# Kernel optimization log

Hardware: AMD Instinct MI355X
Metric: run time of the kernel (lower is better)

Reference implementation:

```python
import jax, jax.numpy as jnp
import numpy as np

N_ETYPES = 6
N_STEPS = 5
N_ITERS = 6
N_LSTM_LAYERS = 3
NODES_PER_GRAPH = 200


def _uinit(key, shape, fan_in):
    s = 1.0 / np.sqrt(fan_in)
    return jax.random.uniform(key, shape, jnp.float32, -s, s)


def setup_inputs() -> dict:
    key = jax.random.key(0)
    ks = jax.random.split(key, 24)
    N, D = 64000, 64
    G = N // NODES_PER_GRAPH  # 320 graphs
    E = N * 16  # 1,024,000 edges
    feats = jax.random.normal(ks[0], (N, D), jnp.float32)
    # within-graph edges: local endpoint + graph offset
    graph_of_edge = jnp.repeat(jnp.arange(G, dtype=jnp.int32), E // G)
    src = jax.random.randint(ks[1], (E,), 0, NODES_PER_GRAPH, jnp.int32) + graph_of_edge * NODES_PER_GRAPH
    dst = jax.random.randint(ks[2], (E,), 0, NODES_PER_GRAPH, jnp.int32) + graph_of_edge * NODES_PER_GRAPH
    etypes = jax.random.randint(ks[3], (E,), 0, N_ETYPES, jnp.int32)
    node_graph = jnp.repeat(jnp.arange(G, dtype=jnp.int32), NODES_PER_GRAPH)
    # GatedGraphConv params: per-etype Linear(D,D) + GRUCell(D,D) (torch gate order r,z,n)
    W_edge = _uinit(ks[4], (N_ETYPES, D, D), D)
    b_edge = _uinit(ks[5], (N_ETYPES, D), D)
    gru_W_ih = _uinit(ks[6], (3 * D, D), D)
    gru_W_hh = _uinit(ks[7], (3 * D, D), D)
    gru_b_ih = _uinit(ks[8], (3 * D,), D)
    gru_b_hh = _uinit(ks[9], (3 * D,), D)
    # Set2Set LSTM: 3 layers, input 2D (layer0) / D (layers 1,2), hidden D; torch gate order i,f,g,o
    lstm_W_ih0 = _uinit(ks[10], (4 * D, 2 * D), D)
    lstm_W_hh0 = _uinit(ks[11], (4 * D, D), D)
    lstm_b_ih0 = _uinit(ks[12], (4 * D,), D)
    lstm_b_hh0 = _uinit(ks[13], (4 * D,), D)
    lstm_W_ih1 = _uinit(ks[14], (4 * D, D), D)
    lstm_W_hh1 = _uinit(ks[15], (4 * D, D), D)
    lstm_b_ih1 = _uinit(ks[16], (4 * D,), D)
    lstm_b_hh1 = _uinit(ks[17], (4 * D,), D)
    lstm_W_ih2 = _uinit(ks[18], (4 * D, D), D)
    lstm_W_hh2 = _uinit(ks[19], (4 * D, D), D)
    lstm_b_ih2 = _uinit(ks[20], (4 * D,), D)
    lstm_b_hh2 = _uinit(ks[21], (4 * D,), D)
    Wp = _uinit(ks[22], (3, 2 * D), 2 * D)
    bp = _uinit(ks[23], (3,), 2 * D)
    return dict(feats=feats, W_edge=W_edge, b_edge=b_edge,
                gru_W_ih=gru_W_ih, gru_W_hh=gru_W_hh, gru_b_ih=gru_b_ih, gru_b_hh=gru_b_hh,
                lstm_W_ih0=lstm_W_ih0, lstm_W_hh0=lstm_W_hh0, lstm_b_ih0=lstm_b_ih0, lstm_b_hh0=lstm_b_hh0,
                lstm_W_ih1=lstm_W_ih1, lstm_W_hh1=lstm_W_hh1, lstm_b_ih1=lstm_b_ih1, lstm_b_hh1=lstm_b_hh1,
                lstm_W_ih2=lstm_W_ih2, lstm_W_hh2=lstm_W_hh2, lstm_b_ih2=lstm_b_ih2, lstm_b_hh2=lstm_b_hh2,
                Wp=Wp, bp=bp, src=src, dst=dst, etypes=etypes, node_graph=node_graph)


def _ggnn_forward(feats, W_edge, b_edge, gru_W_ih, gru_W_hh, gru_b_ih, gru_b_hh,
                  lstm_params, Wp, bp, src, dst, etypes, node_graph):
    N, D = feats.shape
    G = N // NODES_PER_GRAPH
    h = feats
    # --- GatedGraphConv: 5 steps of etype-typed transform + scatter-sum + GRU ---
    for _ in range(N_STEPS):
        # transform every node by every etype weight (cheap: N << E), then gather per edge
        Wh = jnp.einsum('nd,tdo->tno', h, W_edge) + b_edge[:, None, :]  # [T,N,D]
        msg = Wh[etypes, src]                                           # [E,D] gather
        a = jax.ops.segment_sum(msg, dst, num_segments=N)               # [N,D] scatter-add
        gi = a @ gru_W_ih.T + gru_b_ih
        gh = h @ gru_W_hh.T + gru_b_hh
        i_r, i_z, i_n = jnp.split(gi, 3, -1)
        h_r, h_z, h_n = jnp.split(gh, 3, -1)
        r = jax.nn.sigmoid(i_r + h_r)
        z = jax.nn.sigmoid(i_z + h_z)
        n = jnp.tanh(i_n + r * h_n)
        h = (1.0 - z) * n + z * h
    feat = h
    # --- Set2Set readout ---
    q_star = jnp.zeros((G, 2 * D), feat.dtype)
    hs = jnp.zeros((N_LSTM_LAYERS, G, D), feat.dtype)
    cs = jnp.zeros((N_LSTM_LAYERS, G, D), feat.dtype)
    for _ in range(N_ITERS):
        x = q_star
        new_h, new_c = [], []
        for l, (Wi, Whh, bi, bh) in enumerate(lstm_params):
            gates = x @ Wi.T + bi + hs[l] @ Whh.T + bh
            ii, ff, gg, oo = jnp.split(gates, 4, -1)
            c = jax.nn.sigmoid(ff) * cs[l] + jax.nn.sigmoid(ii) * jnp.tanh(gg)
            x = jax.nn.sigmoid(oo) * jnp.tanh(c)
            new_h.append(x)
            new_c.append(c)
        hs = jnp.stack(new_h)
        cs = jnp.stack(new_c)
        q = x  # [G,D]
        e = jnp.sum(feat * q[node_graph], axis=-1)                         # [N]
        emax = jax.ops.segment_max(e, node_graph, num_segments=G)
        ex = jnp.exp(e - emax[node_graph])
        denom = jax.ops.segment_sum(ex, node_graph, num_segments=G)
        alpha = ex / denom[node_graph]                                     # segment softmax
        readout = jax.ops.segment_sum(feat * alpha[:, None], node_graph, num_segments=G)
        q_star = jnp.concatenate([q, readout], axis=-1)
    return q_star @ Wp.T + bp  # [G,3]


def reference(feats, W_edge, b_edge, gru_W_ih, gru_W_hh, gru_b_ih, gru_b_hh,
              lstm_W_ih0, lstm_W_hh0, lstm_b_ih0, lstm_b_hh0,
              lstm_W_ih1, lstm_W_hh1, lstm_b_ih1, lstm_b_hh1,
              lstm_W_ih2, lstm_W_hh2, lstm_b_ih2, lstm_b_hh2,
              Wp, bp, src, dst, etypes, node_graph):
    lstm_params = [
        (lstm_W_ih0, lstm_W_hh0, lstm_b_ih0, lstm_b_hh0),
        (lstm_W_ih1, lstm_W_hh1, lstm_b_ih1, lstm_b_hh1),
        (lstm_W_ih2, lstm_W_hh2, lstm_b_ih2, lstm_b_hh2),
    ]
    return _ggnn_forward(feats, W_edge, b_edge, gru_W_ih, gru_W_hh, gru_b_ih, gru_b_hh,
                         lstm_params, Wp, bp, src, dst, etypes, node_graph)
```

## Files before the change

kernel.cpp:

```cpp
#include <hip/hip_runtime.h>

typedef unsigned short u16;
typedef unsigned int u32;

#define DIM 64
#define NGRAPH 320
#define NPG 200
#define EPG 3200
#define EPG_P 5120
#define NSTEPS 5
#define NITERS 6
#define NTILES 13
#define NPAD 208
#define NTHR 1024

typedef __attribute__((ext_vector_type(8))) short bf16x8;
typedef __attribute__((ext_vector_type(4))) float f32x4;

__device__ __forceinline__ float bf2f(u16 u) {
  u32 x = ((u32)u) << 16;
  float f;
  __builtin_memcpy(&f, &x, 4);
  return f;
}
__device__ __forceinline__ u16 f2bf(float f) {
  u32 x;
  __builtin_memcpy(&x, &f, 4);
  x = (x + 0x7FFFu + ((x >> 16) & 1u)) >> 16;
  return (u16)x;
}
__device__ __forceinline__ float bflo(u32 w) {
  u32 x = w << 16;
  float f;
  __builtin_memcpy(&f, &x, 4);
  return f;
}
__device__ __forceinline__ float bfhi(u32 w) {
  u32 x = w & 0xffff0000u;
  float f;
  __builtin_memcpy(&f, &x, 4);
  return f;
}
__device__ __forceinline__ float sigmf(float x) { return 1.0f / (1.0f + __expf(-x)); }
__device__ __forceinline__ int swz(int row, int col) { return row * 64 + (col ^ ((row & 7) << 3)); }

#define REP13(M) M(0) M(1) M(2) M(3) M(4) M(5) M(6) M(7) M(8) M(9) M(10) M(11) M(12)


__global__ void __launch_bounds__(256) k_csr(const int* __restrict__ src,
                                             const int* __restrict__ dst,
                                             const int* __restrict__ ety,
                                             u16* __restrict__ recs,
                                             int* __restrict__ rows) {
  __shared__ int cnt[3 * NPG];
  __shared__ int rofs[3 * (NPG + 1)];
  int g = blockIdx.x, tid = threadIdx.x;
  int base = g * NPG;
  for (int i = tid; i < 3 * NPG; i += 256) cnt[i] = 0;
  __syncthreads();
  for (int e = tid; e < EPG; e += 256) {
    int d = dst[g * EPG + e] - base;
    int t = ety[g * EPG + e];
    atomicAdd(&cnt[(t >> 1) * NPG + d], 1);
  }
  __syncthreads();
  if (tid == 0) {
    int s = 0;
    for (int p = 0; p < 3; p++) {
      for (int n = 0; n < NPG; n++) {
        rofs[p * (NPG + 1) + n] = s;
        s += (cnt[p * NPG + n] + 3) & ~3;
      }
      rofs[p * (NPG + 1) + NPG] = s;
    }
  }
  __syncthreads();
  for (int i = tid; i < 3 * NPG; i += 256) cnt[i] = rofs[(i / NPG) * (NPG + 1) + (i % NPG)];
  __syncthreads();
  for (int e = tid; e < EPG; e += 256) {
    int d = dst[g * EPG + e] - base;
    int t = ety[g * EPG + e];
    int sl = src[g * EPG + e] - base;
    int pos = atomicAdd(&cnt[(t >> 1) * NPG + d], 1);
    recs[(size_t)g * EPG_P + pos] = (u16)((t & 1) * NPAD + sl);
  }
  __syncthreads();
  for (int i = tid; i < 3 * NPG; i += 256) {
    int ph = i / NPG, n = i % NPG;
    int end = rofs[ph * (NPG + 1) + n + 1];
    for (int p = cnt[i]; p < end; p++) recs[(size_t)g * EPG_P + p] = (u16)NPG;
  }
  for (int i = tid; i < 3 * (NPG + 1); i += 256) rows[g * 3 * (NPG + 1) + i] = rofs[i];
}

__global__ void __launch_bounds__(256) k_prep(
    const float* __restrict__ W_edge, const float* __restrict__ gWih, const float* __restrict__ gWhh,
    const float* __restrict__ lWi0, const float* __restrict__ lWh0,
    const float* __restrict__ lWi1, const float* __restrict__ lWh1,
    const float* __restrict__ lWi2, const float* __restrict__ lWh2,
    u16* __restrict__ WeTb, u16* __restrict__ Wihb, u16* __restrict__ Whhb,
    u16* __restrict__ WTih0b, u16* __restrict__ WThh0b,
    u16* __restrict__ WTih1b, u16* __restrict__ WThh1b,
    u16* __restrict__ WTih2b, u16* __restrict__ WThh2b) {
  int i = blockIdx.x * 256 + threadIdx.x;
  if (i < 24576) {
    int t = i >> 12, rem = i & 4095, o = rem >> 6, k = rem & 63;
    WeTb[i] = f2bf(W_edge[t * 4096 + k * 64 + o]);
  } else if (i < 36864) {
    int idx = i - 24576;
    Wihb[idx] = f2bf(gWih[idx]);
  } else if (i < 49152) {
    int idx = i - 36864;
    Whhb[idx] = f2bf(gWhh[idx]);
  } else if (i < 81920) {
    int idx = i - 49152;
    int k = idx >> 8, jj = idx & 255;
    WTih0b[idx] = f2bf(lWi0[jj * 128 + k]);
  } else {
    int idx = i - 81920;
    int seg = idx >> 14;
    int r = idx & 16383;
    int k = r >> 8, jj = r & 255;
    const float* sp = seg == 0 ? lWh0 : seg == 1 ? lWi1 : seg == 2 ? lWh1 : seg == 3 ? lWi2 : lWh2;
    u16* dp = seg == 0 ? WThh0b : seg == 1 ? WTih1b : seg == 2 ? WThh1b : seg == 3 ? WTih2b : WThh2b;
    dp[r] = f2bf(sp[jj * 64 + k]);
  }
}


__global__ void __launch_bounds__(NTHR) k_ggnn(
    const float* __restrict__ feats,
    const u16* __restrict__ WeTb, const float* __restrict__ b_edge,
    const u16* __restrict__ Wihb, const u16* __restrict__ Whhb,
    const float* __restrict__ gbih, const float* __restrict__ gbhh,
    const u16* __restrict__ recs, const int* __restrict__ rows,
    const u16* __restrict__ WTih0b, const u16* __restrict__ WThh0b,
    const u16* __restrict__ WTih1b, const u16* __restrict__ WThh1b,
    const u16* __restrict__ WTih2b, const u16* __restrict__ WThh2b,
    const float* __restrict__ b_ih0, const float* __restrict__ b_hh0,
    const float* __restrict__ b_ih1, const float* __restrict__ b_hh1,
    const float* __restrict__ b_ih2, const float* __restrict__ b_hh2,
    const float* __restrict__ Wp, const float* __restrict__ bp,
    float* __restrict__ out) {
  __shared__ __align__(16) u16 hb_s[NPAD * 64];
  __shared__ __align__(16) u16 wh_s[2 * NPAD * 64];
  __shared__ __align__(16) float h32_s[NPG * 64];
  __shared__ __align__(16) char u_s[12656];

  u16* rec_s = (u16*)u_s;
  int* rows_s = (int*)(u_s + 10240);
  float* qstar = (float*)u_s;
  float* xbuf = (float*)(u_s + 512);
  float* hs_f = (float*)(u_s + 768);
  float* cs_f = (float*)(u_s + 1536);
  float* gates = (float*)(u_s + 2304);
  float* gpart = (float*)(u_s + 3328);
  float* e_s = (float*)(u_s + 7424);
  float* red_f = (float*)(u_s + 8224);
  float* scal = (float*)(u_s + 12320);

  int g = blockIdx.x, tid = threadIdx.x;
  int lane = tid & 63, wid = tid >> 6;
  int m = lane & 15, quad = lane >> 4;
  int half = lane >> 5, l32 = lane & 31;

  const float* fg = feats + (size_t)g * (NPG * 64);
  for (int i = tid; i < NPG * 64; i += NTHR) {
    float v = fg[i];
    h32_s[i] = v;
    hb_s[swz(i >> 6, i & 63)] = f2bf(v);
  }
  for (int i = tid; i < (NPAD - NPG) * 64; i += NTHR) hb_s[NPG * 64 + i] = 0;
  for (int i = tid; i < 2 * 8 * 64; i += NTHR) {
    int tl = i >> 9, rem = i & 511;
    wh_s[(tl * NPAD + NPG + (rem >> 6)) * 64 + (rem & 63)] = 0;
  }
  {
    const u32* r32 = (const u32*)(recs + (size_t)g * EPG_P);
    u32* rl = (u32*)rec_s;
    for (int i = tid; i < EPG_P / 2; i += NTHR) rl[i] = r32[i];
  }
  for (int i = tid; i < 3 * (NPG + 1); i += NTHR) rows_s[i] = rows[g * 3 * (NPG + 1) + i];

  u16* ab_s = wh_s;
  int ot = wid & 3, hh = wid >> 2;

#define ACC_DECL(q) float a0_##q, a1_##q;
  REP13(ACC_DECL)
#define ACC_ZERO(q) a0_##q = 0.f; a1_##q = 0.f;
#define GATHER(q)                                              \
  {                                                            \
    int n = (q)*16 + wid;                                      \
    if (n < NPG) {                                             \
      int rs = rowp[n], re = rowp[n + 1];                      \
      for (int e = rs; e < re; e += 4) {                       \
        int pA = rec_s[e + half];                              \
        int pB = rec_s[e + 2 + half];                          \
        u32 wA = *(const u32*)(wh_s + pA * 64 + 2 * l32);      \
        u32 wB = *(const u32*)(wh_s + pB * 64 + 2 * l32);      \
        a0_##q += bflo(wA) + bflo(wB);                         \
        a1_##q += bfhi(wA) + bfhi(wB);                         \
      }                                                        \
    }                                                          \
  }
#define FLUSH(q)                                                   \
  {                                                                \
    int n = (q)*16 + wid;                                          \
    float s0 = a0_##q + __shfl_xor(a0_##q, 32);                    \
    float s1 = a1_##q + __shfl_xor(a1_##q, 32);                    \
    if (n < NPG && lane < 32) {                                    \
      u32 pk = (u32)f2bf(s0) | ((u32)f2bf(s1) << 16);              \
      *(u32*)(ab_s + n * 64 + ((2 * l32) ^ ((n & 7) << 3))) = pk;  \
    }                                                              \
  }

#pragma unroll 1
  for (int step = 0; step < NSTEPS; step++) {
    REP13(ACC_ZERO)
#pragma unroll 1
    for (int ph = 0; ph < 3; ph++) {
      __syncthreads();
      {
        const u16* bp0 = WeTb + (((2 * ph) * 64 + ot * 16 + m) * 64) + quad * 8;
        const u16* bp1 = WeTb + (((2 * ph + 1) * 64 + ot * 16 + m) * 64) + quad * 8;
        bf16x8 B00 = *(const bf16x8*)bp0;
        bf16x8 B01 = *(const bf16x8*)(bp0 + 32);
        bf16x8 B10 = *(const bf16x8*)bp1;
        bf16x8 B11 = *(const bf16x8*)(bp1 + 32);
        float bias0 = b_edge[(2 * ph) * 64 + ot * 16 + m];
        float bias1 = b_edge[(2 * ph + 1) * 64 + ot * 16 + m];
        for (int nt = hh; nt < NTILES; nt += 4) {
          int arow = nt * 16 + m;
          bf16x8 a0 = *(const bf16x8*)(hb_s + swz(arow, quad * 8));
          bf16x8 a1 = *(const bf16x8*)(hb_s + swz(arow, quad * 8 + 32));
          f32x4 c = {0.f, 0.f, 0.f, 0.f};
          c = __builtin_amdgcn_mfma_f32_16x16x32_bf16(a0, B00, c, 0, 0, 0);
          c = __builtin_amdgcn_mfma_f32_16x16x32_bf16(a1, B01, c, 0, 0, 0);
#pragma unroll
          for (int r = 0; r < 4; r++) {
            int node = nt * 16 + quad * 4 + r;
            if (node < NPG) wh_s[node * 64 + ot * 16 + m] = f2bf(c[r] + bias0);
          }
        }
        for (int nt = 3 - hh; nt < NTILES; nt += 4) {
          int arow = nt * 16 + m;
          bf16x8 a0 = *(const bf16x8*)(hb_s + swz(arow, quad * 8));
          bf16x8 a1 = *(const bf16x8*)(hb_s + swz(arow, quad * 8 + 32));
          f32x4 c = {0.f, 0.f, 0.f, 0.f};
          c = __builtin_amdgcn_mfma_f32_16x16x32_bf16(a0, B10, c, 0, 0, 0);
          c = __builtin_amdgcn_mfma_f32_16x16x32_bf16(a1, B11, c, 0, 0, 0);
#pragma unroll
          for (int r = 0; r < 4; r++) {
            int node = nt * 16 + quad * 4 + r;
            if (node < NPG) wh_s[(NPAD + node) * 64 + ot * 16 + m] = f2bf(c[r] + bias1);
          }
        }
      }
      __syncthreads();
      const int* rowp = rows_s + ph * (NPG + 1);
      REP13(GATHER)
    }
    __syncthreads();
    REP13(FLUSH)
    __syncthreads();
    if (wid < NTILES) {
      int nt = wid;
      int arow = nt * 16 + m;
      bf16x8 aa0 = *(const bf16x8*)(ab_s + swz(arow, quad * 8));
      bf16x8 aa1 = *(const bf16x8*)(ab_s + swz(arow, quad * 8 + 32));
      bf16x8 ah0 = *(const bf16x8*)(hb_s + swz(arow, quad * 8));
      bf16x8 ah1 = *(const bf16x8*)(hb_s + swz(arow, quad * 8 + 32));
#pragma unroll
      for (int dq = 0; dq < 4; dq++) {
        int d = dq * 16 + m;
        f32x4 z4 = {0.f, 0.f, 0.f, 0.f};
        const u16* bi = Wihb + (dq * 16 + m) * 64 + quad * 8;
        const u16* bh = Whhb + (dq * 16 + m) * 64 + quad * 8;
        f32x4 cr = z4;
        {
          bf16x8 b0 = *(const bf16x8*)bi, b1 = *(const bf16x8*)(bi + 32);
          bf16x8 c0 = *(const bf16x8*)bh, c1 = *(const bf16x8*)(bh + 32);
          cr = __builtin_amdgcn_mfma_f32_16x16x32_bf16(ah0, c0, cr, 0, 0, 0);
          cr = __builtin_amdgcn_mfma_f32_16x16x32_bf16(ah1, c1, cr, 0, 0, 0);
          cr = __builtin_amdgcn_mfma_f32_16x16x32_bf16(aa0, b0, cr, 0, 0, 0);
          cr = __builtin_amdgcn_mfma_f32_16x16x32_bf16(aa1, b1, cr, 0, 0, 0);
        }
        const u16* bi2 = Wihb + ((4 + dq) * 16 + m) * 64 + quad * 8;
        const u16* bh2 = Whhb + ((4 + dq) * 16 + m) * 64 + quad * 8;
        f32x4 cz = z4;
        {
          bf16x8 b0 = *(const bf16x8*)bi2, b1 = *(const bf16x8*)(bi2 + 32);
          bf16x8 c0 = *(const bf16x8*)bh2, c1 = *(const bf16x8*)(bh2 + 32);
          cz = __builtin_amdgcn_mfma_f32_16x16x32_bf16(ah0, c0, cz, 0, 0, 0);
          cz = __builtin_amdgcn_mfma_f32_16x16x32_bf16(ah1, c1, cz, 0, 0, 0);
          cz = __builtin_amdgcn_mfma_f32_16x16x32_bf16(aa0, b0, cz, 0, 0, 0);
          cz = __builtin_amdgcn_mfma_f32_16x16x32_bf16(aa1, b1, cz, 0, 0, 0);
        }
        const u16* bi3 = Wihb + ((8 + dq) * 16 + m) * 64 + quad * 8;
        const u16* bh3 = Whhb + ((8 + dq) * 16 + m) * 64 + quad * 8;
        f32x4 ci = z4, ch = z4;
        {
          bf16x8 b0 = *(const bf16x8*)bi3, b1 = *(const bf16x8*)(bi3 + 32);
          bf16x8 c0 = *(const bf16x8*)bh3, c1 = *(const bf16x8*)(bh3 + 32);
          ci = __builtin_amdgcn_mfma_f32_16x16x32_bf16(aa0, b0, ci, 0, 0, 0);
          ci = __builtin_amdgcn_mfma_f32_16x16x32_bf16(aa1, b1, ci, 0, 0, 0);
          ch = __builtin_amdgcn_mfma_f32_16x16x32_bf16(ah0, c0, ch, 0, 0, 0);
          ch = __builtin_amdgcn_mfma_f32_16x16x32_bf16(ah1, c1, ch, 0, 0, 0);
        }
        float bi_r = gbih[d], bh_r = gbhh[d];
        float bi_z = gbih[64 + d], bh_z = gbhh[64 + d];
        float bi_n = gbih[128 + d], bh_n = gbhh[128 + d];
#pragma unroll
        for (int r = 0; r < 4; r++) {
          int node = nt * 16 + quad * 4 + r;
          if (node < NPG) {
            float rr = sigmf(cr[r] + bi_r + bh_r);
            float zz = sigmf(cz[r] + bi_z + bh_z);
            float nn = tanhf(ci[r] + bi_n + rr * (ch[r] + bh_n));
            float hv = h32_s[node * 64 + d];
            float hnew = (1.0f - zz) * nn + zz * hv;
            h32_s[node * 64 + d] = hnew;
            hb_s[swz(node, d)] = f2bf(hnew);
          }
        }
      }
    }
  }
  __syncthreads();
  const float* feat_s = h32_s;

  int j = tid & 255, part = tid >> 8;
  float bs0 = 0.f, bs1 = 0.f, bs2 = 0.f;
  if (tid < 256) {
    bs0 = b_ih0[tid] + b_hh0[tid];
    bs1 = b_ih1[tid] + b_hh1[tid];
    bs2 = b_ih2[tid] + b_hh2[tid];
  }
  __syncthreads();
  if (tid < 128) qstar[tid] = 0.f;
  if (tid < 64) {
    xbuf[tid] = 0.f;
    for (int l = 0; l < 3; l++) {
      hs_f[l * 64 + tid] = 0.f;
      cs_f[l * 64 + tid] = 0.f;
    }
  }
  __syncthreads();
#pragma unroll 1
  for (int it = 0; it < NITERS; it++) {
    {
      float a0 = 0.f;
      if (part == 0) {
#pragma unroll 8
        for (int k = 0; k < 48; k++) a0 += qstar[k] * bf2f(WTih0b[k * 256 + j]);
      } else if (part == 1) {
#pragma unroll 8
        for (int k = 48; k < 96; k++) a0 += qstar[k] * bf2f(WTih0b[k * 256 + j]);
      } else if (part == 2) {
#pragma unroll 8
        for (int k = 96; k < 128; k++) a0 += qstar[k] * bf2f(WTih0b[k * 256 + j]);
#pragma unroll 8
        for (int k = 0; k < 16; k++) a0 += hs_f[k] * bf2f(WThh0b[k * 256 + j]);
      } else {
#pragma unroll 8
        for (int k = 16; k < 64; k++) a0 += hs_f[k] * bf2f(WThh0b[k * 256 + j]);
      }
      gpart[part * 256 + j] = a0;
    }
    __syncthreads();
    if (tid < 256)
      gates[tid] = gpart[tid] + gpart[256 + tid] + gpart[512 + tid] + gpart[768 + tid] + bs0;
    __syncthreads();
    if (tid < 64) {
      float cc = sigmf(gates[64 + tid]) * cs_f[tid] + sigmf(gates[tid]) * tanhf(gates[128 + tid]);
      float x = sigmf(gates[192 + tid]) * tanhf(cc);
      cs_f[tid] = cc;
      hs_f[tid] = x;
      xbuf[tid] = x;
    }
    __syncthreads();
#pragma unroll 1
    for (int l = 1; l < 3; l++) {
      const u16* W = (l == 1) ? ((part < 2) ? WTih1b : WThh1b)
                              : ((part < 2) ? WTih2b : WThh2b);
      const float* xv = (part < 2) ? xbuf : (hs_f + l * 64);
      int k0 = (part & 1) * 32;
      float a0 = 0.f;
#pragma unroll 8
      for (int k = k0; k < k0 + 32; k++) a0 += xv[k] * bf2f(W[k * 256 + j]);
      gpart[part * 256 + j] = a0;
      __syncthreads();
      float bsl = (l == 1) ? bs1 : bs2;
      if (tid < 256)
        gates[tid] = gpart[tid] + gpart[256 + tid] + gpart[512 + tid] + gpart[768 + tid] + bsl;
      __syncthreads();
      if (tid < 64) {
        float cc = sigmf(gates[64 + tid]) * cs_f[l * 64 + tid] +
                   sigmf(gates[tid]) * tanhf(gates[128 + tid]);
        float x = sigmf(gates[192 + tid]) * tanhf(cc);
        cs_f[l * 64 + tid] = cc;
        hs_f[l * 64 + tid] = x;
        xbuf[tid] = x;
      }
      __syncthreads();
    }
    for (int n = wid; n < NPG; n += 16) {
      float v = feat_s[n * 64 + lane] * xbuf[lane];
      for (int off = 32; off > 0; off >>= 1) v += __shfl_down(v, off);
      if (lane == 0) e_s[n] = v;
    }
    __syncthreads();
    if (tid < 64) {
      float mx = -1e30f;
      for (int n = lane; n < NPG; n += 64) mx = fmaxf(mx, e_s[n]);
      for (int off = 32; off > 0; off >>= 1) mx = fmaxf(mx, __shfl_down(mx, off));
      mx = __shfl(mx, 0);
      float ssum = 0.f;
      for (int n = lane; n < NPG; n += 64) {
        float ex = __expf(e_s[n] - mx);
        e_s[n] = ex;
        ssum += ex;
      }
      for (int off = 32; off > 0; off >>= 1) ssum += __shfl_down(ssum, off);
      if (lane == 0) scal[0] = ssum;
    }
    __syncthreads();
    float denom = scal[0];
    {
      float r = 0.f;
      for (int n = wid; n < NPG; n += 16) r += feat_s[n * 64 + lane] * e_s[n];
      red_f[wid * 64 + lane] = r;
    }
    __syncthreads();
    if (tid < 64) {
      float ro = 0.f;
#pragma unroll
      for (int ww = 0; ww < 16; ww++) ro += red_f[ww * 64 + lane];
      qstar[lane] = xbuf[lane];
      qstar[64 + lane] = ro / denom;
    }
    __syncthreads();
  }
  if (tid < 3) {
    float s = bp[tid];
    for (int k = 0; k < 128; k++) s += qstar[k] * Wp[tid * 128 + k];
    out[g * 3 + tid] = s;
  }
}


extern "C" void kernel_launch(void* const* d_in, const int* in_sizes, int n_in,
                              void* d_out, int out_size, void* d_ws, size_t ws_size,
                              hipStream_t stream) {
  const float* feats  = (const float*)d_in[0];
  const float* W_edge = (const float*)d_in[1];
  const float* b_edge = (const float*)d_in[2];
  const float* gWih   = (const float*)d_in[3];
  const float* gWhh   = (const float*)d_in[4];
  const float* gbih   = (const float*)d_in[5];
  const float* gbhh   = (const float*)d_in[6];
  const float* lWi0   = (const float*)d_in[7];
  const float* lWh0   = (const float*)d_in[8];
  const float* lbi0   = (const float*)d_in[9];
  const float* lbh0   = (const float*)d_in[10];
  const float* lWi1   = (const float*)d_in[11];
  const float* lWh1   = (const float*)d_in[12];
  const float* lbi1   = (const float*)d_in[13];
  const float* lbh1   = (const float*)d_in[14];
  const float* lWi2   = (const float*)d_in[15];
  const float* lWh2   = (const float*)d_in[16];
  const float* lbi2   = (const float*)d_in[17];
  const float* lbh2   = (const float*)d_in[18];
  const float* Wp     = (const float*)d_in[19];
  const float* bp     = (const float*)d_in[20];
  const int* src      = (const int*)d_in[21];
  const int* dst      = (const int*)d_in[22];
  const int* ety      = (const int*)d_in[23];
  float* out = (float*)d_out;

  char* ws = (char*)d_ws;
  u16* recs    = (u16*)ws;
  int* rows    = (int*)(ws + 3276800);
  u16* WeTb    = (u16*)(ws + 4048640);
  u16* Wihb    = (u16*)(ws + 4097792);
  u16* Whhb    = (u16*)(ws + 4122368);
  u16* WTih0b  = (u16*)(ws + 4146944);
  u16* WThh0b  = (u16*)(ws + 4212480);
  u16* WTih1b  = (u16*)(ws + 4245248);
  u16* WThh1b  = (u16*)(ws + 4278016);
  u16* WTih2b  = (u16*)(ws + 4310784);
  u16* WThh2b  = (u16*)(ws + 4343552);

  k_csr<<<NGRAPH, 256, 0, stream>>>(src, dst, ety, recs, rows);
  k_prep<<<640, 256, 0, stream>>>(W_edge, gWih, gWhh, lWi0, lWh0, lWi1, lWh1, lWi2, lWh2,
                                  WeTb, Wihb, Whhb, WTih0b, WThh0b, WTih1b, WThh1b, WTih2b, WThh2b);
  k_ggnn<<<NGRAPH, NTHR, 0, stream>>>(feats, WeTb, b_edge, Wihb, Whhb, gbih, gbhh, recs, rows,
                                      WTih0b, WThh0b, WTih1b, WThh1b, WTih2b, WThh2b,
                                      lbi0, lbh0, lbi1, lbh1, lbi2, lbh2, Wp, bp, out);
}
```

Before: 706.0 us.

## Replace CSR gather aggregation with dense per-etype adjacency MFMA

Builds per-graph, per-edge-type dense adjacency count matrices packed as 4-bit nibbles in MFMA fragment order, using atomics in a simple per-edge kernel. Message aggregation becomes a bf16 MFMA of the adjacency with the transformed hidden states, replacing the LDS gather loops over CSR records. The edge-linear stage is also rebalanced across all 16 waves and writes a transposed Wh layout. The cost is a large workspace memset plus a global adjacency read every step. Nibble counts overflow if more than 15 parallel edges share a (dst, src, type) triple.

```diff
diff --git a/kernel.cpp b/kernel.cpp
--- a/kernel.cpp
+++ b/kernel.cpp
@@ -2,17 +2,21 @@
 
 typedef unsigned short u16;
 typedef unsigned int u32;
+typedef unsigned char u8;
+typedef unsigned long long u64;
 
 #define DIM 64
 #define NGRAPH 320
 #define NPG 200
 #define EPG 3200
-#define EPG_P 5120
+#define NEDGE (NGRAPH * EPG)
 #define NSTEPS 5
 #define NITERS 6
 #define NTILES 13
 #define NPAD 208
 #define NTHR 1024
+#define AFRAGS 91
+#define ADJ_PG (6 * AFRAGS * 256)
 
 typedef __attribute__((ext_vector_type(8))) short bf16x8;
 typedef __attribute__((ext_vector_type(4))) float f32x4;
@@ -29,68 +33,34 @@
   x = (x + 0x7FFFu + ((x >> 16) & 1u)) >> 16;
   return (u16)x;
 }
-__device__ __forceinline__ float bflo(u32 w) {
-  u32 x = w << 16;
-  float f;
-  __builtin_memcpy(&f, &x, 4);
-  return f;
-}
-__device__ __forceinline__ float bfhi(u32 w) {
-  u32 x = w & 0xffff0000u;
-  float f;
-  __builtin_memcpy(&f, &x, 4);
-  return f;
-}
 __device__ __forceinline__ float sigmf(float x) { return 1.0f / (1.0f + __expf(-x)); }
 __device__ __forceinline__ int swz(int row, int col) { return row * 64 + (col ^ ((row & 7) << 3)); }
 
-#define REP13(M) M(0) M(1) M(2) M(3) M(4) M(5) M(6) M(7) M(8) M(9) M(10) M(11) M(12)
-
-
-__global__ void __launch_bounds__(256) k_csr(const int* __restrict__ src,
+__device__ __forceinline__ bf16x8 nib2bf(u32 w) {
+  union { u16 u[8]; bf16x8 v; } r;
+#pragma unroll
+  for (int i = 0; i < 8; i++) {
+    float f = (float)((w >> (4 * i)) & 15u);
+    u32 b;
+    __builtin_memcpy(&b, &f, 4);
+    r.u[i] = (u16)(b >> 16);
+  }
+  return r.v;
+}
+
+
+__global__ void __launch_bounds__(256) k_adj(const int* __restrict__ src,
                                              const int* __restrict__ dst,
                                              const int* __restrict__ ety,
-                                             u16* __restrict__ recs,
-                                             int* __restrict__ rows) {
-  __shared__ int cnt[3 * NPG];
-  __shared__ int rofs[3 * (NPG + 1)];
-  int g = blockIdx.x, tid = threadIdx.x;
+                                             u8* __restrict__ adj) {
+  int e = blockIdx.x * 256 + threadIdx.x;
+  if (e >= NEDGE) return;
+  int g = e / EPG;
   int base = g * NPG;
-  for (int i = tid; i < 3 * NPG; i += 256) cnt[i] = 0;
-  __syncthreads();
-  for (int e = tid; e < EPG; e += 256) {
-    int d = dst[g * EPG + e] - base;
-    int t = ety[g * EPG + e];
-    atomicAdd(&cnt[(t >> 1) * NPG + d], 1);
-  }
-  __syncthreads();
-  if (tid == 0) {
-    int s = 0;
-    for (int p = 0; p < 3; p++) {
-      for (int n = 0; n < NPG; n++) {
-        rofs[p * (NPG + 1) + n] = s;
-        s += (cnt[p * NPG + n] + 3) & ~3;
-      }
-      rofs[p * (NPG + 1) + NPG] = s;
-    }
-  }
-  __syncthreads();
-  for (int i = tid; i < 3 * NPG; i += 256) cnt[i] = rofs[(i / NPG) * (NPG + 1) + (i % NPG)];
-  __syncthreads();
-  for (int e = tid; e < EPG; e += 256) {
-    int d = dst[g * EPG + e] - base;
-    int t = ety[g * EPG + e];
-    int sl = src[g * EPG + e] - base;
-    int pos = atomicAdd(&cnt[(t >> 1) * NPG + d], 1);
-    recs[(size_t)g * EPG_P + pos] = (u16)((t & 1) * NPAD + sl);
-  }
-  __syncthreads();
-  for (int i = tid; i < 3 * NPG; i += 256) {
-    int ph = i / NPG, n = i % NPG;
-    int end = rofs[ph * (NPG + 1) + n + 1];
-    for (int p = cnt[i]; p < end; p++) recs[(size_t)g * EPG_P + p] = (u16)NPG;
-  }
-  for (int i = tid; i < 3 * (NPG + 1); i += 256) rows[g * 3 * (NPG + 1) + i] = rofs[i];
+  int d = dst[e] - base, s = src[e] - base, t = ety[e];
+  int nt = d >> 4, m = d & 15, kc = s >> 5, quad = (s >> 3) & 3, nib = s & 7;
+  u32 word = ((u32)(g * 6 + t) * AFRAGS + nt * 7 + kc) * 64 + quad * 16 + m;
+  atomicAdd((u32*)adj + word, 1u << (4 * nib));
 }
 
 __global__ void __launch_bounds__(256) k_prep(
@@ -133,7 +103,7 @@
     const u16* __restrict__ WeTb, const float* __restrict__ b_edge,
     const u16* __restrict__ Wihb, const u16* __restrict__ Whhb,
     const float* __restrict__ gbih, const float* __restrict__ gbhh,
-    const u16* __restrict__ recs, const int* __restrict__ rows,
+    const u8* __restrict__ adj,
     const u16* __restrict__ WTih0b, const u16* __restrict__ WThh0b,
     const u16* __restrict__ WTih1b, const u16* __restrict__ WThh1b,
     const u16* __restrict__ WTih2b, const u16* __restrict__ WThh2b,
@@ -143,12 +113,10 @@
     const float* __restrict__ Wp, const float* __restrict__ bp,
     float* __restrict__ out) {
   __shared__ __align__(16) u16 hb_s[NPAD * 64];
-  __shared__ __align__(16) u16 wh_s[2 * NPAD * 64];
+  __shared__ __align__(16) u16 whT[2 * 64 * 256];
   __shared__ __align__(16) float h32_s[NPG * 64];
-  __shared__ __align__(16) char u_s[12656];
-
-  u16* rec_s = (u16*)u_s;
-  int* rows_s = (int*)(u_s + 10240);
+  __shared__ __align__(16) char u_s[12328];
+
   float* qstar = (float*)u_s;
   float* xbuf = (float*)(u_s + 512);
   float* hs_f = (float*)(u_s + 768);
@@ -162,7 +130,6 @@
   int g = blockIdx.x, tid = threadIdx.x;
   int lane = tid & 63, wid = tid >> 6;
   int m = lane & 15, quad = lane >> 4;
-  int half = lane >> 5, l32 = lane & 31;
 
   const float* fg = feats + (size_t)g * (NPG * 64);
   for (int i = tid; i < NPG * 64; i += NTHR) {
@@ -171,97 +138,80 @@
     hb_s[swz(i >> 6, i & 63)] = f2bf(v);
   }
   for (int i = tid; i < (NPAD - NPG) * 64; i += NTHR) hb_s[NPG * 64 + i] = 0;
-  for (int i = tid; i < 2 * 8 * 64; i += NTHR) {
-    int tl = i >> 9, rem = i & 511;
-    wh_s[(tl * NPAD + NPG + (rem >> 6)) * 64 + (rem & 63)] = 0;
-  }
   {
-    const u32* r32 = (const u32*)(recs + (size_t)g * EPG_P);
-    u32* rl = (u32*)rec_s;
-    for (int i = tid; i < EPG_P / 2; i += NTHR) rl[i] = r32[i];
-  }
-  for (int i = tid; i < 3 * (NPG + 1); i += NTHR) rows_s[i] = rows[g * 3 * (NPG + 1) + i];
-
-  u16* ab_s = wh_s;
-  int ot = wid & 3, hh = wid >> 2;
-
-#define ACC_DECL(q) float a0_##q, a1_##q;
-  REP13(ACC_DECL)
-#define ACC_ZERO(q) a0_##q = 0.f; a1_##q = 0.f;
-#define GATHER(q)                                              \
-  {                                                            \
-    int n = (q)*16 + wid;                                      \
-    if (n < NPG) {                                             \
-      int rs = rowp[n], re = rowp[n + 1];                      \
-      for (int e = rs; e < re; e += 4) {                       \
-        int pA = rec_s[e + half];                              \
-        int pB = rec_s[e + 2 + half];                          \
-        u32 wA = *(const u32*)(wh_s + pA * 64 + 2 * l32);      \
-        u32 wB = *(const u32*)(wh_s + pB * 64 + 2 * l32);      \
-        a0_##q += bflo(wA) + bflo(wB);                         \
-        a1_##q += bfhi(wA) + bfhi(wB);                         \
-      }                                                        \
-    }                                                          \
-  }
-#define FLUSH(q)                                                   \
-  {                                                                \
-    int n = (q)*16 + wid;                                          \
-    float s0 = a0_##q + __shfl_xor(a0_##q, 32);                    \
-    float s1 = a1_##q + __shfl_xor(a1_##q, 32);                    \
-    if (n < NPG && lane < 32) {                                    \
-      u32 pk = (u32)f2bf(s0) | ((u32)f2bf(s1) << 16);              \
-      *(u32*)(ab_s + n * 64 + ((2 * l32) ^ ((n & 7) << 3))) = pk;  \
-    }                                                              \
-  }
+    u32* wz = (u32*)whT;
+    for (int i = tid; i < 2 * 64 * 128; i += NTHR) wz[i] = 0;
+  }
+  const u8* adjg = adj + (size_t)g * ADJ_PG;
+  u16* ab_s = whT;
+  int mm = (m & 7) << 3;
+
+  __syncthreads();
 
 #pragma unroll 1
   for (int step = 0; step < NSTEPS; step++) {
-    REP13(ACC_ZERO)
+    f32x4 cg0 = {0.f, 0.f, 0.f, 0.f}, cg1 = cg0, cg2 = cg0, cg3 = cg0;
 #pragma unroll 1
     for (int ph = 0; ph < 3; ph++) {
       __syncthreads();
-      {
-        const u16* bp0 = WeTb + (((2 * ph) * 64 + ot * 16 + m) * 64) + quad * 8;
-        const u16* bp1 = WeTb + (((2 * ph + 1) * 64 + ot * 16 + m) * 64) + quad * 8;
-        bf16x8 B00 = *(const bf16x8*)bp0;
-        bf16x8 B01 = *(const bf16x8*)(bp0 + 32);
-        bf16x8 B10 = *(const bf16x8*)bp1;
-        bf16x8 B11 = *(const bf16x8*)(bp1 + 32);
-        float bias0 = b_edge[(2 * ph) * 64 + ot * 16 + m];
-        float bias1 = b_edge[(2 * ph + 1) * 64 + ot * 16 + m];
-        for (int nt = hh; nt < NTILES; nt += 4) {
-          int arow = nt * 16 + m;
-          bf16x8 a0 = *(const bf16x8*)(hb_s + swz(arow, quad * 8));
-          bf16x8 a1 = *(const bf16x8*)(hb_s + swz(arow, quad * 8 + 32));
-          f32x4 c = {0.f, 0.f, 0.f, 0.f};
-          c = __builtin_amdgcn_mfma_f32_16x16x32_bf16(a0, B00, c, 0, 0, 0);
-          c = __builtin_amdgcn_mfma_f32_16x16x32_bf16(a1, B01, c, 0, 0, 0);
-#pragma unroll
-          for (int r = 0; r < 4; r++) {
-            int node = nt * 16 + quad * 4 + r;
-            if (node < NPG) wh_s[node * 64 + ot * 16 + m] = f2bf(c[r] + bias0);
+      for (int j = wid; j < 104; j += 16) {
+        int tl = j >= 52 ? 1 : 0;
+        int rem = j - tl * 52;
+        int otj = rem / 13, ntj = rem - otj * 13;
+        int t = 2 * ph + tl;
+        int row = otj * 16 + m;
+        const u16* bp_ = WeTb + (t * 64 + row) * 64 + quad * 8;
+        bf16x8 B0 = *(const bf16x8*)bp_;
+        bf16x8 B1 = *(const bf16x8*)(bp_ + 32);
+        int arow = ntj * 16 + m;
+        bf16x8 a0 = *(const bf16x8*)(hb_s + swz(arow, quad * 8));
+        bf16x8 a1 = *(const bf16x8*)(hb_s + swz(arow, quad * 8 + 32));
+        f32x4 c = {0.f, 0.f, 0.f, 0.f};
+        c = __builtin_amdgcn_mfma_f32_16x16x32_bf16(a0, B0, c, 0, 0, 0);
+        c = __builtin_amdgcn_mfma_f32_16x16x32_bf16(a1, B1, c, 0, 0, 0);
+        float bias = b_edge[t * 64 + row];
+        u16 p0 = f2bf(c[0] + bias), p1 = f2bf(c[1] + bias);
+        u16 p2 = f2bf(c[2] + bias), p3 = f2bf(c[3] + bias);
+        u64 pk = (u64)p0 | ((u64)p1 << 16) | ((u64)p2 << 32) | ((u64)p3 << 48);
+        int colbase = ntj * 16 + quad * 4;
+        *(u64*)(whT + tl * 16384 + row * 256 + (colbase ^ ((row & 7) << 3))) = pk;
+      }
+      __syncthreads();
+      if (wid < NTILES) {
+#pragma unroll 1
+        for (int tl = 0; tl < 2; tl++) {
+          const u8* ap = adjg + ((size_t)((2 * ph + tl) * AFRAGS + wid * 7)) * 256 + lane * 4;
+          const u16* wt = whT + tl * 16384;
+#pragma unroll
+          for (int kc = 0; kc < 7; kc++) {
+            u32 w = *(const u32*)(ap + kc * 256);
+            bf16x8 af = nib2bf(w);
+            int cb = kc * 32 + quad * 8;
+            bf16x8 b0 = *(const bf16x8*)(wt + (0 * 16 + m) * 256 + (cb ^ mm));
+            cg0 = __builtin_amdgcn_mfma_f32_16x16x32_bf16(af, b0, cg0, 0, 0, 0);
+            bf16x8 b1 = *(const bf16x8*)(wt + (1 * 16 + m) * 256 + (cb ^ mm));
+            cg1 = __builtin_amdgcn_mfma_f32_16x16x32_bf16(af, b1, cg1, 0, 0, 0);
+            bf16x8 b2 = *(const bf16x8*)(wt + (2 * 16 + m) * 256 + (cb ^ mm));
+            cg2 = __builtin_amdgcn_mfma_f32_16x16x32_bf16(af, b2, cg2, 0, 0, 0);
+            bf16x8 b3 = *(const bf16x8*)(wt + (3 * 16 + m) * 256 + (cb ^ mm));
+            cg3 = __builtin_amdgcn_mfma_f32_16x16x32_bf16(af, b3, cg3, 0, 0, 0);
           }
         }
-        for (int nt = 3 - hh; nt < NTILES; nt += 4) {
-          int arow = nt * 16 + m;
-          bf16x8 a0 = *(const bf16x8*)(hb_s + swz(arow, quad * 8));
-          bf16x8 a1 = *(const bf16x8*)(hb_s + swz(arow, quad * 8 + 32));
-          f32x4 c = {0.f, 0.f, 0.f, 0.f};
-          c = __builtin_amdgcn_mfma_f32_16x16x32_bf16(a0, B10, c, 0, 0, 0);
-          c = __builtin_amdgcn_mfma_f32_16x16x32_bf16(a1, B11, c, 0, 0, 0);
-#pragma unroll
-          for (int r = 0; r < 4; r++) {
-            int node = nt * 16 + quad * 4 + r;
-            if (node < NPG) wh_s[(NPAD + node) * 64 + ot * 16 + m] = f2bf(c[r] + bias1);
-          }
-        }
-      }
-      __syncthreads();
-      const int* rowp = rows_s + ph * (NPG + 1);
-      REP13(GATHER)
-    }
-    __syncthreads();
-    REP13(FLUSH)
+      }
+    }
+    __syncthreads();
+    if (wid < NTILES) {
+#pragma unroll
+      for (int r = 0; r < 4; r++) {
+        int node = wid * 16 + quad * 4 + r;
+        if (node < NPG) {
+          ab_s[swz(node, 0 * 16 + m)] = f2bf(cg0[r]);
+          ab_s[swz(node, 1 * 16 + m)] = f2bf(cg1[r]);
+          ab_s[swz(node, 2 * 16 + m)] = f2bf(cg2[r]);
+          ab_s[swz(node, 3 * 16 + m)] = f2bf(cg3[r]);
+        }
+      }
+    }
     __syncthreads();
     if (wid < NTILES) {
       int nt = wid;
@@ -336,7 +286,6 @@
     bs1 = b_ih1[tid] + b_hh1[tid];
     bs2 = b_ih2[tid] + b_hh2[tid];
   }
-  __syncthreads();
   if (tid < 128) qstar[tid] = 0.f;
   if (tid < 64) {
     xbuf[tid] = 0.f;
@@ -479,22 +428,22 @@
   float* out = (float*)d_out;
 
   char* ws = (char*)d_ws;
-  u16* recs    = (u16*)ws;
-  int* rows    = (int*)(ws + 3276800);
-  u16* WeTb    = (u16*)(ws + 4048640);
-  u16* Wihb    = (u16*)(ws + 4097792);
-  u16* Whhb    = (u16*)(ws + 4122368);
-  u16* WTih0b  = (u16*)(ws + 4146944);
-  u16* WThh0b  = (u16*)(ws + 4212480);
-  u16* WTih1b  = (u16*)(ws + 4245248);
-  u16* WThh1b  = (u16*)(ws + 4278016);
-  u16* WTih2b  = (u16*)(ws + 4310784);
-  u16* WThh2b  = (u16*)(ws + 4343552);
-
-  k_csr<<<NGRAPH, 256, 0, stream>>>(src, dst, ety, recs, rows);
+  u8* adjb = (u8*)ws;
+  u16* WeTb    = (u16*)(ws + 44728320);
+  u16* Wihb    = (u16*)(ws + 44777472);
+  u16* Whhb    = (u16*)(ws + 44802048);
+  u16* WTih0b  = (u16*)(ws + 44826624);
+  u16* WThh0b  = (u16*)(ws + 44892160);
+  u16* WTih1b  = (u16*)(ws + 44924928);
+  u16* WThh1b  = (u16*)(ws + 44957696);
+  u16* WTih2b  = (u16*)(ws + 44990464);
+  u16* WThh2b  = (u16*)(ws + 45023232);
+
+  hipMemsetAsync(adjb, 0, (size_t)NGRAPH * ADJ_PG, stream);
+  k_adj<<<(NEDGE + 255) / 256, 256, 0, stream>>>(src, dst, ety, adjb);
   k_prep<<<640, 256, 0, stream>>>(W_edge, gWih, gWhh, lWi0, lWh0, lWi1, lWh1, lWi2, lWh2,
                                   WeTb, Wihb, Whhb, WTih0b, WThh0b, WTih1b, WThh1b, WTih2b, WThh2b);
-  k_ggnn<<<NGRAPH, NTHR, 0, stream>>>(feats, WeTb, b_edge, Wihb, Whhb, gbih, gbhh, recs, rows,
+  k_ggnn<<<NGRAPH, NTHR, 0, stream>>>(feats, WeTb, b_edge, Wihb, Whhb, gbih, gbhh, adjb,
                                       WTih0b, WThh0b, WTih1b, WThh1b, WTih2b, WThh2b,
                                       lbi0, lbh0, lbi1, lbh1, lbi2, lbh2, Wp, bp, out);
 }
```

New measurement: 879.2 us. 1.25x slower.
